# Performance work log

Measured on AMD Instinct MI355X. Metric: run time of the kernel, lower is better.

Reference implementation:

```python
import jax, jax.numpy as jnp
import numpy as np

N = 100_000      # nodes
E = 800_000      # edges per edge type
T = 3            # num_edge_types - 1 relation-specific convs
D_IN = 128
D_OUT = 128


def setup_inputs() -> dict:
    key = jax.random.key(0)
    k1, k2, k3, k4 = jax.random.split(key, 4)
    x = jax.random.normal(k1, (N, D_IN), dtype=jnp.float32)
    edges = jax.random.randint(k2, (T, 2, E), 0, N, dtype=jnp.int32)
    W = jax.random.normal(k3, (T, D_IN, D_OUT), dtype=jnp.float32) * (1.0 / np.sqrt(D_IN))
    b = jax.random.normal(k4, (T, D_OUT), dtype=jnp.float32) * 0.02
    return {"x": x, "edges": edges, "W": W, "b": b}


def _gcn_conv(x, ei, W, b):
    """PyG GCNConv: add self-loops, symmetric D^-1/2 (A+I) D^-1/2 norm, XW, +b."""
    n = x.shape[0]
    xw = x @ W                                   # [N, D_OUT]
    loop = jnp.arange(n, dtype=ei.dtype)
    src = jnp.concatenate([ei[0], loop])         # [E+N]
    dst = jnp.concatenate([ei[1], loop])         # [E+N]
    deg = jax.ops.segment_sum(jnp.ones(src.shape[0], xw.dtype), dst, num_segments=n)
    dis = jnp.where(deg > 0, jax.lax.rsqrt(jnp.maximum(deg, 1e-12)), 0.0)
    norm = dis[src] * dis[dst]                   # [E+N]
    msg = xw[src] * norm[:, None]                # gather-transform: [E+N, D_OUT]
    out = jax.ops.segment_sum(msg, dst, num_segments=n)  # scatter-add back to nodes
    return out + b


def reference(x, edges, W, b):
    # Sum of per-edge-type GCN convolutions into a shared output buffer.
    out = jnp.zeros((x.shape[0], W.shape[-1]), dtype=x.dtype)
    for i in range(edges.shape[0]):              # small fixed relation loop
        out = out + _gcn_conv(x, edges[i], W[i], b[i])
    return out
```

## Files before the change

### kernel.cpp

```cpp
#include <hip/hip_runtime.h>

#define NN 100000
#define EE 800000
#define TT 3
#define D  128
#define NB 391
#define CAPB 7168
#define CHUNK 8192
#define LSTRIDE 392
#define ENC 32767.0f

typedef unsigned short bf16_t;

typedef __bf16 bf16x8_t __attribute__((ext_vector_type(8)));
typedef float  f32x4_t  __attribute__((ext_vector_type(4)));

union ABFrag { bf16x8_t v; uint4 q; };

__device__ __forceinline__ bf16_t f2bf(float f) {
    unsigned u = __float_as_uint(f);
    u += 0x7fff + ((u >> 16) & 1);
    return (bf16_t)(u >> 16);
}
__device__ __forceinline__ float bf_lo(unsigned p) { return __uint_as_float(p << 16); }
__device__ __forceinline__ float bf_hi(unsigned p) { return __uint_as_float(p & 0xFFFF0000u); }

__global__ void quant_kernel(const float* __restrict__ x, bf16_t* __restrict__ xq) {
    int i = (blockIdx.x * 256 + threadIdx.x) * 4;
    if (i >= NN * D) return;
    float4 f = *(const float4*)(x + i);
    uint2 p;
    p.x = (unsigned)f2bf(f.x) | ((unsigned)f2bf(f.y) << 16);
    p.y = (unsigned)f2bf(f.z) | ((unsigned)f2bf(f.w) << 16);
    *(uint2*)(xq + i) = p;
}

__global__ void wconv_kernel(const float* __restrict__ W, bf16_t* __restrict__ WT) {
    int t = blockIdx.y, n = blockIdx.x, k = threadIdx.x;
    WT[((size_t)t * D + n) * D + k] = f2bf(W[((size_t)t * D + k) * D + n]);
}

__global__ __launch_bounds__(512, 4) void bin_kernel(const int* __restrict__ edges,
                                                     int* __restrict__ bcnt,
                                                     unsigned* __restrict__ bin) {
    __shared__ int hist[NB];
    __shared__ int lbase[NB];
    __shared__ int gbase[NB];
    __shared__ int scn[512];
    __shared__ unsigned srec[CHUNK];
    __shared__ unsigned stgt[CHUNK];
    int tid = threadIdx.x;
    int t = blockIdx.y;
    int f0 = blockIdx.x * CHUNK;
    const int* sb = edges + (size_t)t * 2 * EE;
    const int* db = sb + EE;

    for (int i = tid; i < NB; i += 512) hist[i] = 0;
    __syncthreads();

    int4 s4[4], d4[4];
    int rnk[16];
    bool have[4];
#pragma unroll
    for (int j = 0; j < 4; ++j) {
        int e = f0 + ((j * 512 + tid) << 2);
        have[j] = (e < EE);
        if (have[j]) { s4[j] = *(const int4*)(sb + e); d4[j] = *(const int4*)(db + e); }
    }
#pragma unroll
    for (int j = 0; j < 4; ++j) {
        if (have[j]) {
            rnk[j * 4 + 0] = atomicAdd(&hist[d4[j].x >> 8], 1);
            rnk[j * 4 + 1] = atomicAdd(&hist[d4[j].y >> 8], 1);
            rnk[j * 4 + 2] = atomicAdd(&hist[d4[j].z >> 8], 1);
            rnk[j * 4 + 3] = atomicAdd(&hist[d4[j].w >> 8], 1);
        }
    }
    __syncthreads();

    int hv = (tid < NB) ? hist[tid] : 0;
    scn[tid] = hv;
    __syncthreads();
    for (int off = 1; off < 512; off <<= 1) {
        int u = 0;
        if (tid >= off) u = scn[tid - off];
        __syncthreads();
        if (tid >= off) scn[tid] += u;
        __syncthreads();
    }
    if (tid < NB) {
        lbase[tid] = scn[tid] - hv;
        gbase[tid] = (hv > 0) ? atomicAdd(&bcnt[tid], hv) : 0;
    }
    __syncthreads();

#pragma unroll
    for (int j = 0; j < 4; ++j) {
        if (have[j]) {
            int ss[4] = {s4[j].x, s4[j].y, s4[j].z, s4[j].w};
            int dd[4] = {d4[j].x, d4[j].y, d4[j].z, d4[j].w};
#pragma unroll
            for (int k = 0; k < 4; ++k) {
                int bkt = dd[k] >> 8;
                int r = rnk[j * 4 + k];
                int pos = lbase[bkt] + r;
                int rel = gbase[bkt] + r;
                srec[pos] = ((unsigned)(dd[k] & 255) << 19) | ((unsigned)t << 17) | (unsigned)ss[k];
                stgt[pos] = (rel < CAPB) ? (unsigned)(bkt * CAPB + rel) : 0xFFFFFFFFu;
            }
        }
    }
    __syncthreads();

    int nval = EE - f0; if (nval > CHUNK) nval = CHUNK;
    for (int i = tid; i < nval; i += 512) {
        unsigned tg = stgt[i];
        if (tg != 0xFFFFFFFFu) bin[tg] = srec[i];
    }
}

#define MAXR 14
__global__ __launch_bounds__(512) void sort_kernel(const int* __restrict__ bcnt,
                                                   unsigned* __restrict__ bin,
                                                   float* __restrict__ dis3,
                                                   int* __restrict__ cnts3,
                                                   int* __restrict__ nodeoff) {
    __shared__ int cnt[768];
    __shared__ int tot[256];
    int tid = threadIdx.x;
    int b = blockIdx.x;
    int c = bcnt[b]; if (c > CAPB) c = CAPB;
    unsigned* reg = bin + (size_t)b * CAPB;

    for (int i = tid; i < 768; i += 512) cnt[i] = 0;
    __syncthreads();

    unsigned ur[MAXR];
    int rr[MAXR];
    bool vld[MAXR];
#pragma unroll
    for (int k = 0; k < MAXR; ++k) {
        int i = tid + k * 512;
        vld[k] = (i < c);
        unsigned u = vld[k] ? reg[i] : 0u;
        ur[k] = u;
        int bi = (int)(u >> 19) * 3 + (int)((u >> 17) & 3);
        rr[k] = vld[k] ? atomicAdd(&cnt[bi], 1) : 0;
    }
    __syncthreads();

    int d0 = 0, d1 = 0, d2 = 0;
    if (tid < 256) {
        d0 = cnt[tid * 3]; d1 = cnt[tid * 3 + 1]; d2 = cnt[tid * 3 + 2];
        tot[tid] = d0 + d1 + d2;
    }
    __syncthreads();
    for (int off = 1; off < 256; off <<= 1) {
        int v = 0;
        if (tid < 256 && tid >= off) v = tot[tid - off];
        __syncthreads();
        if (tid < 256 && tid >= off) tot[tid] += v;
        __syncthreads();
    }
    if (tid < 256) {
        int excl = tot[tid] - (d0 + d1 + d2);
        int gnode = b * 256 + tid;
        if (gnode < NN) {
            nodeoff[gnode] = b * CAPB + excl;
            cnts3[gnode]   = d0 | (d1 << 8) | (d2 << 16);
            dis3[gnode]            = rsqrtf((float)d0 + 1.f);
            dis3[NN + gnode]       = rsqrtf((float)d1 + 1.f);
            dis3[2 * NN + gnode]   = rsqrtf((float)d2 + 1.f);
        }
        cnt[tid * 3]     = excl;
        cnt[tid * 3 + 1] = excl + d0;
        cnt[tid * 3 + 2] = excl + d0 + d1;
    }
    __syncthreads();
#pragma unroll
    for (int k = 0; k < MAXR; ++k) {
        if (vld[k]) {
            unsigned u = ur[k];
            int bi = (int)(u >> 19) * 3 + (int)((u >> 17) & 3);
            reg[cnt[bi] + rr[k]] = u & 0x7FFFFu;
        }
    }
}

__global__ __launch_bounds__(512) void weightize_kernel(const int* __restrict__ bcnt,
                                                        const float* __restrict__ dis3,
                                                        unsigned* __restrict__ bin) {
    int b = blockIdx.x;
    int c = bcnt[b]; if (c > CAPB) c = CAPB;
    unsigned* reg = bin + (size_t)b * CAPB;
    for (int i = threadIdx.x; i < c; i += 512) {
        unsigned u = reg[i];
        unsigned src = u & 0x1FFFFu;
        unsigned t = (u >> 17) & 3u;
        float w = dis3[t * NN + src];
        reg[i] = ((unsigned)(w * ENC + 0.5f) << 17) | src;
    }
}


#define ISSUE(UX, SA, J0)                                                          \
    {                                                                              \
        const int _j0 = (J0);                                                      \
        _Pragma("unroll")                                                          \
        for (int k = 0; k < 8; ++k) {                                              \
            SA[k] = __builtin_amdgcn_readlane((int)uw, _j0 + k);                   \
            int sxk = SA[k] & 0x1FFFF;                                             \
            UX[k] = *(const unsigned*)(xq + (size_t)sxk * D + (lane << 1));        \
        }                                                                          \
    }

#define CONSUME(UX, SA, J0)                                                        \
    {                                                                              \
        const int _j0 = (J0);                                                      \
        _Pragma("unroll")                                                          \
        for (int k = 0; k < 8; ++k) {                                              \
            int idxk = _j0 + k;                                                    \
            float wk = (float)(((unsigned)SA[k]) >> 17);                           \
            unsigned u = UX[k];                                                    \
            float xl = bf_lo(u), xh = bf_hi(u);                                    \
            if (idxk < b1S)      { a00 += wk * xl; a01 += wk * xh; }               \
            else if (idxk < b2S) { a10 += wk * xl; a11 += wk * xh; }               \
            else                 { a20 += wk * xl; a21 += wk * xh; }               \
        }                                                                          \
    }

__global__ __launch_bounds__(1024, 8) void fused_kernel(const bf16_t* __restrict__ xq,
                                                        const float* __restrict__ dis3,
                                                        const int* __restrict__ cnts3,
                                                        const int* __restrict__ nodeoff,
                                                        const unsigned* __restrict__ recs,
                                                        const bf16_t* __restrict__ WT,
                                                        const float* __restrict__ bias,
                                                        float* __restrict__ out) {
    __shared__ __attribute__((aligned(16))) ushort ylds[16 * LSTRIDE];
    int tid  = threadIdx.x;
    int lane = tid & 63;
    int wave = tid >> 6;
    int n0 = blockIdx.x * 16;
    int n  = n0 + wave;

    unsigned su = *(const unsigned*)(xq + (size_t)n * D + (lane << 1));
    float xs0 = bf_lo(su), xs1 = bf_hi(su);

    float dn0 = dis3[n], dn1 = dis3[NN + n], dn2 = dis3[2 * NN + n];
    int pk = cnts3[n];
    int d0 = pk & 255, d1 = (pk >> 8) & 255, d2 = (pk >> 16) & 255;
    int s0 = nodeoff[n];

    int b1S = __builtin_amdgcn_readfirstlane(d0);
    int b2S = __builtin_amdgcn_readfirstlane(d0 + d1);
    int cT  = d0 + d1 + d2; if (cT > 64) cT = 64;
    int cS  = __builtin_amdgcn_readfirstlane(cT);

    unsigned uraw = recs[s0 + lane];
    unsigned uw = (lane < cS) ? uraw : 0u;

    float a00 = dn0 * ENC * xs0, a01 = dn0 * ENC * xs1;
    float a10 = dn1 * ENC * xs0, a11 = dn1 * ENC * xs1;
    float a20 = dn2 * ENC * xs0, a21 = dn2 * ENC * xs1;

    unsigned uxA[8], uxB[8];
    int sA[8], sB[8];

    if (cS > 0) {
        int nb = (cS + 7) >> 3;
        ISSUE(uxA, sA, 0)
        int blk = 0;
        while (true) {
            if (blk + 1 < nb) ISSUE(uxB, sB, (blk + 1) * 8)
            CONSUME(uxA, sA, blk * 8)
            if (++blk >= nb) break;
            if (blk + 1 < nb) ISSUE(uxA, sA, (blk + 1) * 8)
            CONSUME(uxB, sB, blk * 8)
            if (++blk >= nb) break;
        }
    }

    {
        float f0 = dn0 * (1.0f / ENC), f1 = dn1 * (1.0f / ENC), f2 = dn2 * (1.0f / ENC);
        a00 *= f0; a01 *= f0; a10 *= f1; a11 *= f1; a20 *= f2; a21 *= f2;
        ushort* yw = ylds + wave * LSTRIDE + (lane << 1);
        *(unsigned*)(yw)         = (unsigned)f2bf(a00) | ((unsigned)f2bf(a01) << 16);
        *(unsigned*)(yw + D)     = (unsigned)f2bf(a10) | ((unsigned)f2bf(a11) << 16);
        *(unsigned*)(yw + 2 * D) = (unsigned)f2bf(a20) | ((unsigned)f2bf(a21) << 16);
    }
    __syncthreads();

    if (wave < 8) {
        int quad = lane >> 4;
        int lid  = lane & 15;
        int col  = wave * 16 + lid;
        f32x4_t acc = {0.f, 0.f, 0.f, 0.f};
        const ushort* yr = ylds + lid * LSTRIDE;
#pragma unroll
        for (int t = 0; t < TT; ++t) {
            const bf16_t* wn = WT + ((size_t)t * D + col) * D;
#pragma unroll
            for (int s = 0; s < 4; ++s) {
                ABFrag av, bv;
                av.q = *(const uint4*)(yr + t * D + s * 32 + quad * 8);
                bv.q = *(const uint4*)(wn + s * 32 + quad * 8);
                acc = __builtin_amdgcn_mfma_f32_16x16x32_bf16(av.v, bv.v, acc, 0, 0, 0);
            }
        }
        float bc = bias[col] + bias[D + col] + bias[2 * D + col];
#pragma unroll
        for (int r = 0; r < 4; ++r)
            out[(size_t)(n0 + quad * 4 + r) * D + col] = acc[r] + bc;
    }
}

extern "C" void kernel_launch(void* const* d_in, const int* in_sizes, int n_in,
                              void* d_out, int out_size, void* d_ws, size_t ws_size,
                              hipStream_t stream) {
    const float* x     = (const float*)d_in[0];
    const int*   edges = (const int*)d_in[1];
    const float* W     = (const float*)d_in[2];
    const float* b     = (const float*)d_in[3];
    float*       out   = (float*)d_out;

    char* w = (char*)d_ws;
    bf16_t*   xq      = (bf16_t*)w;
    unsigned* bin     = (unsigned*)(w + (size_t)NN * D * 2);
    float*    dis3    = (float*)((char*)bin + (size_t)NB * CAPB * 4);
    int*      cnts3   = (int*)((char*)dis3 + (size_t)3 * NN * 4);
    int*      nodeoff = cnts3 + NN;
    bf16_t*   WT      = (bf16_t*)(nodeoff + NN);
    int*      bcnt    = (int*)((char*)WT + (size_t)TT * D * D * 2);

    hipMemsetAsync(bcnt, 0, (size_t)NB * sizeof(int), stream);

    quant_kernel<<<(NN * D / 4 + 255) / 256, 256, 0, stream>>>(x, xq);
    {
        dim3 g(D, TT);
        wconv_kernel<<<g, D, 0, stream>>>(W, WT);
    }

    {
        dim3 g((EE + CHUNK - 1) / CHUNK, TT);
        bin_kernel<<<g, 512, 0, stream>>>(edges, bcnt, bin);
    }

    sort_kernel<<<NB, 512, 0, stream>>>(bcnt, bin, dis3, cnts3, nodeoff);

    weightize_kernel<<<NB, 512, 0, stream>>>(bcnt, dis3, bin);

    fused_kernel<<<NN / 16, 1024, 0, stream>>>(xq, dis3, cnts3, nodeoff, bin, WT, b, out);
}
```

Before: 313.2 us.

## Process two nodes per wave in fused kernel with 512-thread blocks

Each wave now aggregates two destination nodes, interleaving their gather/accumulate pipelines, and the block shrinks from 16 to 8 waves. All 8 waves then take part in the MFMA projection stage, where previously half of them sat idle. The intent is more memory-level parallelism per wave, since two nodes' gathers are in flight at once, and no idle waves after the barrier. The cost is higher register pressure from doubled accumulators and buffers, and fewer resident threads per block.

```diff
diff --git a/kernel.cpp b/kernel.cpp
--- a/kernel.cpp
+++ b/kernel.cpp
@@ -203,18 +203,18 @@
 }
 
 
-#define ISSUE(UX, SA, J0)                                                          \
+#define ISSUE(UX, SA, UW, J0)                                                      \
     {                                                                              \
         const int _j0 = (J0);                                                      \
         _Pragma("unroll")                                                          \
         for (int k = 0; k < 8; ++k) {                                              \
-            SA[k] = __builtin_amdgcn_readlane((int)uw, _j0 + k);                   \
+            SA[k] = __builtin_amdgcn_readlane((int)(UW), _j0 + k);                 \
             int sxk = SA[k] & 0x1FFFF;                                             \
             UX[k] = *(const unsigned*)(xq + (size_t)sxk * D + (lane << 1));        \
         }                                                                          \
     }
 
-#define CONSUME(UX, SA, J0)                                                        \
+#define CONSUME(UX, SA, J0, B1, B2, A00, A01, A10, A11, A20, A21)                  \
     {                                                                              \
         const int _j0 = (J0);                                                      \
         _Pragma("unroll")                                                          \
@@ -223,75 +223,94 @@
             float wk = (float)(((unsigned)SA[k]) >> 17);                           \
             unsigned u = UX[k];                                                    \
             float xl = bf_lo(u), xh = bf_hi(u);                                    \
-            if (idxk < b1S)      { a00 += wk * xl; a01 += wk * xh; }               \
-            else if (idxk < b2S) { a10 += wk * xl; a11 += wk * xh; }               \
-            else                 { a20 += wk * xl; a21 += wk * xh; }               \
+            if (idxk < B1)      { A00 += wk * xl; A01 += wk * xh; }                \
+            else if (idxk < B2) { A10 += wk * xl; A11 += wk * xh; }                \
+            else                { A20 += wk * xl; A21 += wk * xh; }                \
         }                                                                          \
     }
 
-__global__ __launch_bounds__(1024, 8) void fused_kernel(const bf16_t* __restrict__ xq,
-                                                        const float* __restrict__ dis3,
-                                                        const int* __restrict__ cnts3,
-                                                        const int* __restrict__ nodeoff,
-                                                        const unsigned* __restrict__ recs,
-                                                        const bf16_t* __restrict__ WT,
-                                                        const float* __restrict__ bias,
-                                                        float* __restrict__ out) {
+__global__ __launch_bounds__(512, 8) void fused_kernel(const bf16_t* __restrict__ xq,
+                                                       const float* __restrict__ dis3,
+                                                       const int* __restrict__ cnts3,
+                                                       const int* __restrict__ nodeoff,
+                                                       const unsigned* __restrict__ recs,
+                                                       const bf16_t* __restrict__ WT,
+                                                       const float* __restrict__ bias,
+                                                       float* __restrict__ out) {
     __shared__ __attribute__((aligned(16))) ushort ylds[16 * LSTRIDE];
     int tid  = threadIdx.x;
     int lane = tid & 63;
     int wave = tid >> 6;
     int n0 = blockIdx.x * 16;
-    int n  = n0 + wave;
-
-    unsigned su = *(const unsigned*)(xq + (size_t)n * D + (lane << 1));
-    float xs0 = bf_lo(su), xs1 = bf_hi(su);
-
-    float dn0 = dis3[n], dn1 = dis3[NN + n], dn2 = dis3[2 * NN + n];
-    int pk = cnts3[n];
-    int d0 = pk & 255, d1 = (pk >> 8) & 255, d2 = (pk >> 16) & 255;
-    int s0 = nodeoff[n];
-
-    int b1S = __builtin_amdgcn_readfirstlane(d0);
-    int b2S = __builtin_amdgcn_readfirstlane(d0 + d1);
-    int cT  = d0 + d1 + d2; if (cT > 64) cT = 64;
-    int cS  = __builtin_amdgcn_readfirstlane(cT);
-
-    unsigned uraw = recs[s0 + lane];
-    unsigned uw = (lane < cS) ? uraw : 0u;
-
-    float a00 = dn0 * ENC * xs0, a01 = dn0 * ENC * xs1;
-    float a10 = dn1 * ENC * xs0, a11 = dn1 * ENC * xs1;
-    float a20 = dn2 * ENC * xs0, a21 = dn2 * ENC * xs1;
+    int nA = n0 + wave * 2;
+    int nB = nA + 1;
+
+    unsigned suA = *(const unsigned*)(xq + (size_t)nA * D + (lane << 1));
+    unsigned suB = *(const unsigned*)(xq + (size_t)nB * D + (lane << 1));
+    float dnA0 = dis3[nA], dnA1 = dis3[NN + nA], dnA2 = dis3[2 * NN + nA];
+    float dnB0 = dis3[nB], dnB1 = dis3[NN + nB], dnB2 = dis3[2 * NN + nB];
+    int pkA = cnts3[nA], pkB = cnts3[nB];
+    int s0A = nodeoff[nA], s0B = nodeoff[nB];
+
+    int dA0 = pkA & 255, dA1 = (pkA >> 8) & 255, dA2 = (pkA >> 16) & 255;
+    int dB0 = pkB & 255, dB1 = (pkB >> 8) & 255, dB2 = (pkB >> 16) & 255;
+
+    int b1A = __builtin_amdgcn_readfirstlane(dA0);
+    int b2A = __builtin_amdgcn_readfirstlane(dA0 + dA1);
+    int cTA = dA0 + dA1 + dA2; if (cTA > 64) cTA = 64;
+    int cSA = __builtin_amdgcn_readfirstlane(cTA);
+    int b1B = __builtin_amdgcn_readfirstlane(dB0);
+    int b2B = __builtin_amdgcn_readfirstlane(dB0 + dB1);
+    int cTB = dB0 + dB1 + dB2; if (cTB > 64) cTB = 64;
+    int cSB = __builtin_amdgcn_readfirstlane(cTB);
+
+    unsigned uwA = recs[s0A + lane]; if (lane >= cSA) uwA = 0u;
+    unsigned uwB = recs[s0B + lane]; if (lane >= cSB) uwB = 0u;
+
+    float xsA0 = bf_lo(suA), xsA1 = bf_hi(suA);
+    float xsB0 = bf_lo(suB), xsB1 = bf_hi(suB);
+
+    float aA00 = dnA0 * ENC * xsA0, aA01 = dnA0 * ENC * xsA1;
+    float aA10 = dnA1 * ENC * xsA0, aA11 = dnA1 * ENC * xsA1;
+    float aA20 = dnA2 * ENC * xsA0, aA21 = dnA2 * ENC * xsA1;
+    float aB00 = dnB0 * ENC * xsB0, aB01 = dnB0 * ENC * xsB1;
+    float aB10 = dnB1 * ENC * xsB0, aB11 = dnB1 * ENC * xsB1;
+    float aB20 = dnB2 * ENC * xsB0, aB21 = dnB2 * ENC * xsB1;
 
     unsigned uxA[8], uxB[8];
     int sA[8], sB[8];
 
-    if (cS > 0) {
-        int nb = (cS + 7) >> 3;
-        ISSUE(uxA, sA, 0)
-        int blk = 0;
-        while (true) {
-            if (blk + 1 < nb) ISSUE(uxB, sB, (blk + 1) * 8)
-            CONSUME(uxA, sA, blk * 8)
-            if (++blk >= nb) break;
-            if (blk + 1 < nb) ISSUE(uxA, sA, (blk + 1) * 8)
-            CONSUME(uxB, sB, blk * 8)
-            if (++blk >= nb) break;
+    int nbA = (cSA + 7) >> 3;
+    int nbB = (cSB + 7) >> 3;
+    if (nbA > 0) ISSUE(uxA, sA, uwA, 0)
+    if (nbB > 0) ISSUE(uxB, sB, uwB, 0)
+    int nbmax = nbA > nbB ? nbA : nbB;
+    for (int blk = 0; blk < nbmax; ++blk) {
+        if (blk < nbA) {
+            CONSUME(uxA, sA, blk * 8, b1A, b2A, aA00, aA01, aA10, aA11, aA20, aA21)
+            if (blk + 1 < nbA) ISSUE(uxA, sA, uwA, (blk + 1) * 8)
+        }
+        if (blk < nbB) {
+            CONSUME(uxB, sB, blk * 8, b1B, b2B, aB00, aB01, aB10, aB11, aB20, aB21)
+            if (blk + 1 < nbB) ISSUE(uxB, sB, uwB, (blk + 1) * 8)
         }
     }
 
     {
-        float f0 = dn0 * (1.0f / ENC), f1 = dn1 * (1.0f / ENC), f2 = dn2 * (1.0f / ENC);
-        a00 *= f0; a01 *= f0; a10 *= f1; a11 *= f1; a20 *= f2; a21 *= f2;
-        ushort* yw = ylds + wave * LSTRIDE + (lane << 1);
-        *(unsigned*)(yw)         = (unsigned)f2bf(a00) | ((unsigned)f2bf(a01) << 16);
-        *(unsigned*)(yw + D)     = (unsigned)f2bf(a10) | ((unsigned)f2bf(a11) << 16);
-        *(unsigned*)(yw + 2 * D) = (unsigned)f2bf(a20) | ((unsigned)f2bf(a21) << 16);
-    }
-    __syncthreads();
-
-    if (wave < 8) {
+        float fA0 = dnA0 * (1.0f / ENC), fA1 = dnA1 * (1.0f / ENC), fA2 = dnA2 * (1.0f / ENC);
+        float fB0 = dnB0 * (1.0f / ENC), fB1 = dnB1 * (1.0f / ENC), fB2 = dnB2 * (1.0f / ENC);
+        ushort* ywA = ylds + (wave * 2) * LSTRIDE + (lane << 1);
+        ushort* ywB = ywA + LSTRIDE;
+        *(unsigned*)(ywA)         = (unsigned)f2bf(aA00 * fA0) | ((unsigned)f2bf(aA01 * fA0) << 16);
+        *(unsigned*)(ywA + D)     = (unsigned)f2bf(aA10 * fA1) | ((unsigned)f2bf(aA11 * fA1) << 16);
+        *(unsigned*)(ywA + 2 * D) = (unsigned)f2bf(aA20 * fA2) | ((unsigned)f2bf(aA21 * fA2) << 16);
+        *(unsigned*)(ywB)         = (unsigned)f2bf(aB00 * fB0) | ((unsigned)f2bf(aB01 * fB0) << 16);
+        *(unsigned*)(ywB + D)     = (unsigned)f2bf(aB10 * fB1) | ((unsigned)f2bf(aB11 * fB1) << 16);
+        *(unsigned*)(ywB + 2 * D) = (unsigned)f2bf(aB20 * fB2) | ((unsigned)f2bf(aB21 * fB2) << 16);
+    }
+    __syncthreads();
+
+    {
         int quad = lane >> 4;
         int lid  = lane & 15;
         int col  = wave * 16 + lid;
@@ -350,5 +369,5 @@
 
     weightize_kernel<<<NB, 512, 0, stream>>>(bcnt, dis3, bin);
 
-    fused_kernel<<<NN / 16, 1024, 0, stream>>>(xq, dis3, cnts3, nodeoff, bin, WT, b, out);
-}
+    fused_kernel<<<NN / 16, 512, 0, stream>>>(xq, dis3, cnts3, nodeoff, bin, WT, b, out);
+}
```

After: 304.5 us. -2.8%, faster.
